# Performance work log

Measured on AMD Instinct MI355X. Metric: run time of the kernel, lower is better.

The kernel has to match this reference:

```python
import jax, jax.numpy as jnp
import numpy as np

D_STATE = 16
D_CONV = 4
EXPAND = 2
GROUPS = 8
EPS = 1e-5


def _layernorm(x, w, b):
    m = x.mean(-1, keepdims=True)
    v = x.var(-1, keepdims=True)
    return (x - m) * jax.lax.rsqrt(v + EPS) * w + b


def _groupnorm(x, w, b):
    B, C = x.shape[:2]
    sp = x.shape[2:]
    xg = x.reshape(B, GROUPS, C // GROUPS, -1)
    m = xg.mean(axis=(2, 3), keepdims=True)
    v = xg.var(axis=(2, 3), keepdims=True)
    xg = (xg - m) * jax.lax.rsqrt(v + EPS)
    x = xg.reshape((B, C) + sp)
    shp = (1, C) + (1,) * len(sp)
    return x * w.reshape(shp) + b.reshape(shp)


def _mamba(xn, in_w, conv_w, conv_b, xp_w, dt_w, dt_b, A_log, Dp, out_w):
    # xn: [B, L, C]
    B, L, C = xn.shape
    di = in_w.shape[0] // 2
    rank = dt_w.shape[1]
    N = D_STATE
    xz = xn @ in_w.T                              # [B, L, 2*di]
    xi, z = xz[..., :di], xz[..., di:]
    # causal depthwise conv1d along L (pad left d_conv-1, truncate to L)
    xc = jnp.moveaxis(xi, 1, 2)                   # [B, di, L]
    xpd = jnp.pad(xc, ((0, 0), (0, 0), (D_CONV - 1, 0)))
    conv = conv_b[None, :, None]
    for k in range(D_CONV):
        conv = conv + conv_w[None, :, k, None] * xpd[:, :, k:k + L]
    u = jnp.moveaxis(jax.nn.silu(conv), 1, 2)     # [B, L, di]
    dbl = u @ xp_w.T                              # [B, L, rank+2N]
    dt = dbl[..., :rank]
    Bm = dbl[..., rank:rank + N]
    Cm = dbl[..., rank + N:]
    delta = jax.nn.softplus(dt @ dt_w.T + dt_b)   # [B, L, di]
    A = -jnp.exp(A_log)                           # [di, N]
    dA = jnp.exp(delta[..., None] * A)            # [B, L, di, N]
    dBu = delta[..., None] * Bm[:, :, None, :] * u[..., None]

    def comb(e1, e2):
        a1, b1 = e1
        a2, b2 = e2
        return a1 * a2, a2 * b1 + b2

    _, h = jax.lax.associative_scan(comb, (dA, dBu), axis=1)  # h_t = dA_t*h_{t-1} + dBu_t
    y = jnp.einsum('bldn,bln->bld', h, Cm) + u * Dp
    y = y * jax.nn.silu(z)
    return y @ out_w.T


def _mamba_layer(x, p):
    B, C = x.shape[:2]
    img = x.shape[2:]
    L = int(np.prod(img))
    xf = jnp.moveaxis(x.reshape(B, C, L), 1, 2)   # [B, L, C]
    xn = _layernorm(xf, p['ln_w'], p['ln_b'])
    xm = _mamba(xn, p['in_w'], p['conv_w'], p['conv_b'], p['xp_w'],
                p['dt_w'], p['dt_b'], p['A_log'], p['Dp'], p['out_w'])
    xm = xm + p['skip'] * xf
    xm = _layernorm(xm, p['ln_w'], p['ln_b'])     # same norm params reused, as in source
    y = xm @ p['proj_w'].T + p['proj_b']
    return jnp.moveaxis(y, 1, 2).reshape((B, C) + img)


def setup_inputs() -> dict:
    key = jax.random.key(0)
    B, C = 2, 48
    img = (16, 32, 32)
    di = EXPAND * C
    rank = -(-C // 16)
    ks = iter(jax.random.split(key, 64))

    def nrm(shape, scale):
        return jax.random.normal(next(ks), shape, jnp.float32) * scale

    inp = {'x': jax.random.normal(next(ks), (B, C) + img, jnp.float32)}
    inp['gn1_w'] = jnp.ones(C); inp['gn1_b'] = jnp.zeros(C)
    inp['gn2_w'] = jnp.ones(C); inp['gn2_b'] = jnp.zeros(C)
    for i in (1, 2):
        inp[f'ln{i}_w'] = jnp.ones(C); inp[f'ln{i}_b'] = jnp.zeros(C)
        inp[f'in_w{i}'] = nrm((2 * di, C), C ** -0.5)
        inp[f'conv_w{i}'] = nrm((di, D_CONV), D_CONV ** -0.5)
        inp[f'conv_b{i}'] = jnp.zeros(di)
        inp[f'xp_w{i}'] = nrm((rank + 2 * D_STATE, di), di ** -0.5)
        inp[f'dt_w{i}'] = nrm((di, rank), rank ** -0.5)
        inp[f'dt_b{i}'] = nrm((di,), 0.1) - 4.0  # softplus -> small positive dt
        inp[f'A_log{i}'] = jnp.log(jnp.tile(jnp.arange(1, D_STATE + 1, dtype=jnp.float32), (di, 1)))
        inp[f'D{i}'] = jnp.ones(di)
        inp[f'out_w{i}'] = nrm((C, di), di ** -0.5)
        inp[f'proj_w{i}'] = nrm((C, C), C ** -0.5)
        inp[f'proj_b{i}'] = jnp.zeros(C)
        inp[f'skip{i}'] = jnp.ones(1)
    return inp


def reference(x, gn1_w, gn1_b, gn2_w, gn2_b,
              ln1_w, ln1_b, in_w1, conv_w1, conv_b1, xp_w1, dt_w1, dt_b1, A_log1, D1, out_w1, proj_w1, proj_b1, skip1,
              ln2_w, ln2_b, in_w2, conv_w2, conv_b2, xp_w2, dt_w2, dt_b2, A_log2, D2, out_w2, proj_w2, proj_b2, skip2):
    p1 = dict(ln_w=ln1_w, ln_b=ln1_b, in_w=in_w1, conv_w=conv_w1, conv_b=conv_b1, xp_w=xp_w1,
              dt_w=dt_w1, dt_b=dt_b1, A_log=A_log1, Dp=D1, out_w=out_w1, proj_w=proj_w1,
              proj_b=proj_b1, skip=skip1)
    p2 = dict(ln_w=ln2_w, ln_b=ln2_b, in_w=in_w2, conv_w=conv_w2, conv_b=conv_b2, xp_w=xp_w2,
              dt_w=dt_w2, dt_b=dt_b2, A_log=A_log2, Dp=D2, out_w=out_w2, proj_w=proj_w2,
              proj_b=proj_b2, skip=skip2)
    identity = x
    h = jax.nn.relu(_groupnorm(x, gn1_w, gn1_b))
    h = _mamba_layer(h, p1)
    h = jax.nn.relu(_groupnorm(h, gn2_w, gn2_b))
    h = _mamba_layer(h, p2)
    return h + identity
```

## Files before the change

### kernel.cpp

```cpp
#include <hip/hip_runtime.h>
#include <hip/hip_bf16.h>

#define LCH   48
#define DI    96
#define LSEQ  16384
#define NB    2
#define NPOS  (NB*LSEQ)
#define NSTATE 16
#define CPG   6
#define EPS   1e-5f
#define NC    128
#define CL    128
#define NCHAIN (NB*DI*NSTATE)
#define TS    32

typedef __hip_bfloat16 bf16;

__device__ __forceinline__ float LDW(const void* p, size_t i, bool f32){
    return f32 ? ((const float*)p)[i] : __bfloat162float(((const bf16*)p)[i]);
}

__device__ __forceinline__ float bf2f(unsigned short h){
    union { unsigned int i; float f; } u; u.i = ((unsigned int)h) << 16; return u.f;
}

__device__ __forceinline__ float4 LDW4(const void* p, size_t i4, bool f32){
    if (f32) return ((const float4*)p)[i4];
    ushort4 v = ((const ushort4*)p)[i4];
    return make_float4(bf2f(v.x), bf2f(v.y), bf2f(v.z), bf2f(v.w));
}

__device__ __forceinline__ float row16_sum(float p){
    union { float f; int i; } u, v;
    u.f = p; v.i = __builtin_amdgcn_mov_dpp(u.i, 0x111, 0xf, 0xf, true); p += v.f;
    u.f = p; v.i = __builtin_amdgcn_mov_dpp(u.i, 0x112, 0xf, 0xf, true); p += v.f;
    u.f = p; v.i = __builtin_amdgcn_mov_dpp(u.i, 0x114, 0xf, 0xf, true); p += v.f;
    u.f = p; v.i = __builtin_amdgcn_mov_dpp(u.i, 0x118, 0xf, 0xf, true); p += v.f;
    return p;
}

__global__ void k_flag(const void* gnw, int* flag){
    const unsigned short* g = (const unsigned short*)gnw;
    flag[0] = (g[0] == 0x3F80) ? 0 : 1;
}

__global__ void k_gnzero(float* __restrict__ acc){
    int t = threadIdx.x;
    if (t < 32) acc[t] = 0.f;
}

__global__ void k_gnpart_x(const void* __restrict__ x, const int* Fg, float* __restrict__ acc){
    const bool f32 = Fg[0];
    int bg = blockIdx.x >> 4, sl = blockIdx.x & 15;
    int b = bg >> 3, g = bg & 7;
    int tid = threadIdx.x;
    float s = 0.f, q = 0.f;
    for (int c = 0; c < CPG; ++c){
        size_t base = (size_t)(b*LCH + g*CPG + c)*LSEQ + sl*1024;
        for (int l = tid; l < 1024; l += 256){ float v = LDW(x, base + l, f32); s += v; q += v*v; }
    }
    __shared__ float ss[256], sq[256];
    ss[tid] = s; sq[tid] = q; __syncthreads();
    for (int st = 128; st > 0; st >>= 1){
        if (tid < st){ ss[tid] += ss[tid+st]; sq[tid] += sq[tid+st]; }
        __syncthreads();
    }
    if (tid == 0){
        atomicAdd(&acc[bg*2],   ss[0]);
        atomicAdd(&acc[bg*2+1], sq[0]);
    }
}

__global__ void k_gnpart_m(const float* __restrict__ m, float* __restrict__ acc){
    int bg = blockIdx.x >> 4, sl = blockIdx.x & 15;
    int b = bg >> 3, g = bg & 7;
    int tid = threadIdx.x;
    float s = 0.f, q = 0.f;
    for (int i = tid; i < 1024*CPG; i += 256){
        int l = sl*1024 + i/CPG, c = i % CPG;
        float v = m[(size_t)(b*LSEQ + l)*LCH + g*CPG + c];
        s += v; q += v*v;
    }
    __shared__ float ss[256], sq[256];
    ss[tid] = s; sq[tid] = q; __syncthreads();
    for (int st = 128; st > 0; st >>= 1){
        if (tid < st){ ss[tid] += ss[tid+st]; sq[tid] += sq[tid+st]; }
        __syncthreads();
    }
    if (tid == 0){
        atomicAdd(&acc[bg*2],   ss[0]);
        atomicAdd(&acc[bg*2+1], sq[0]);
    }
}

__global__ void k_gnfin(const float* __restrict__ acc, float* __restrict__ stats){
    int t = threadIdx.x;
    if (t < 16){
        float mean = acc[t*2] / (float)(CPG*LSEQ);
        float var  = acc[t*2+1] / (float)(CPG*LSEQ) - mean*mean;
        stats[t*2]   = mean;
        stats[t*2+1] = rsqrtf(var + EPS);
    }
}

__global__ void k_prep_x(const void* __restrict__ x, const int* Fg, const float* __restrict__ stats,
                         const void* gnw, const void* gnb, const void* lnw, const void* lnb,
                         float* __restrict__ xf, float* __restrict__ xn){
    const bool f32 = Fg[0];
    __shared__ float xl[128*49];
    __shared__ float fl[128*49];
    int tid = threadIdx.x;
    int pos0 = blockIdx.x*128;
    int b = pos0 >> 14, l0 = pos0 & (LSEQ-1);
    for (int i = tid; i < 48*128; i += 256){
        int c = i >> 7, p = i & 127;
        xl[p*49+c] = LDW(x, (size_t)(b*LCH+c)*LSEQ + l0 + p, f32);
    }
    __syncthreads();
    if (tid < 128){
        float* row  = xl + tid*49;
        float* frow = fl + tid*49;
        float s = 0.f, q = 0.f;
        #pragma unroll
        for (int c = 0; c < LCH; ++c){
            int g = c / CPG;
            float mean = stats[(b*8+g)*2], rs = stats[(b*8+g)*2+1];
            float v = row[c];
            v = (v - mean)*rs*LDW(gnw,c,f32) + LDW(gnb,c,f32);
            v = fmaxf(v, 0.f);
            frow[c] = v; s += v; q += v*v;
        }
        float mean = s / (float)LCH;
        float rs = rsqrtf(q/(float)LCH - mean*mean + EPS);
        #pragma unroll
        for (int c = 0; c < LCH; ++c)
            row[c] = (frow[c]-mean)*rs*LDW(lnw,c,f32) + LDW(lnb,c,f32);
    }
    __syncthreads();
    for (int i = tid; i < 128*48; i += 256){
        int p = i/48, c = i - p*48;
        xf[(size_t)pos0*LCH + i] = fl[p*49+c];
        xn[(size_t)pos0*LCH + i] = xl[p*49+c];
    }
}

__global__ void k_prep_m(const float* __restrict__ msrc, const int* Fg, const float* __restrict__ stats,
                         const void* gnw, const void* gnb, const void* lnw, const void* lnb,
                         float* __restrict__ xf, float* __restrict__ xn){
    const bool f32 = Fg[0];
    __shared__ float xl[128*49];
    __shared__ float fl[128*49];
    int tid = threadIdx.x;
    int pos0 = blockIdx.x*128;
    int b = pos0 >> 14;
    for (int i = tid; i < 128*48; i += 256){
        int p = i/48, c = i - p*48;
        xl[p*49+c] = msrc[(size_t)pos0*LCH + i];
    }
    __syncthreads();
    if (tid < 128){
        float* row  = xl + tid*49;
        float* frow = fl + tid*49;
        float s = 0.f, q = 0.f;
        #pragma unroll
        for (int c = 0; c < LCH; ++c){
            int g = c / CPG;
            float mean = stats[(b*8+g)*2], rs = stats[(b*8+g)*2+1];
            float v = row[c];
            v = (v - mean)*rs*LDW(gnw,c,f32) + LDW(gnb,c,f32);
            v = fmaxf(v, 0.f);
            frow[c] = v; s += v; q += v*v;
        }
        float mean = s / (float)LCH;
        float rs = rsqrtf(q/(float)LCH - mean*mean + EPS);
        #pragma unroll
        for (int c = 0; c < LCH; ++c)
            row[c] = (frow[c]-mean)*rs*LDW(lnw,c,f32) + LDW(lnb,c,f32);
    }
    __syncthreads();
    for (int i = tid; i < 128*48; i += 256){
        int p = i/48, c = i - p*48;
        xf[(size_t)pos0*LCH + i] = fl[p*49+c];
        xn[(size_t)pos0*LCH + i] = xl[p*49+c];
    }
}

__global__ void k_inproj(const float* __restrict__ xn, const void* __restrict__ inw, const int* Fg,
                         float* __restrict__ xi, float* __restrict__ z){
    const bool f32 = Fg[0];
    __shared__ float wl[192*50];
    __shared__ float xl[32*48];
    int pos0 = blockIdx.x*32;
    for (int i = threadIdx.x; i < 192*48; i += 256){
        int o = i/48, k = i - o*48;
        wl[o*50+k] = LDW(inw, i, f32);
    }
    for (int i = threadIdx.x; i < 32*48; i += 256)
        xl[i] = xn[(size_t)pos0*LCH + i];
    __syncthreads();
    int os = threadIdx.x & 63;
    int pofs = threadIdx.x >> 6;
    #pragma unroll
    for (int j = 0; j < 2; ++j){
        int p0 = pofs + j*16;
        float a0[4] = {0.f,0.f,0.f,0.f};
        float a1[4] = {0.f,0.f,0.f,0.f};
        float a2[4] = {0.f,0.f,0.f,0.f};
        #pragma unroll 4
        for (int k = 0; k < 48; ++k){
            float w0 = wl[ os      *50+k];
            float w1 = wl[(os+64 ) *50+k];
            float w2 = wl[(os+128) *50+k];
            #pragma unroll
            for (int q = 0; q < 4; ++q){
                float xv = xl[(p0+q*4)*48+k];
                a0[q] += xv*w0; a1[q] += xv*w1; a2[q] += xv*w2;
            }
        }
        #pragma unroll
        for (int q = 0; q < 4; ++q){
            int pos = pos0 + p0 + q*4;
            xi[(size_t)pos*DI + os] = a0[q];
            if (os < 32) xi[(size_t)pos*DI + 64 + os] = a1[q];
            else         z [(size_t)pos*DI + (os-32)] = a1[q];
            z[(size_t)pos*DI + (os+32)] = a2[q];
        }
    }
}

__global__ void k_convdbl(const float* __restrict__ xi, const void* cw, const void* cb,
                          const void* __restrict__ xpw, const void* dtw, const void* dtb,
                          const int* Fg, float* __restrict__ u_g, float* __restrict__ BC2,
                          float* __restrict__ delta_g){
    const bool f32 = Fg[0];
    __shared__ float xil[35*100];
    __shared__ float wbc[32*97];
    __shared__ float wdt[3*97];
    __shared__ float cwl[96*4];
    __shared__ float cbl[96];
    __shared__ float dtwl[96*3];
    __shared__ float dtbl[96];
    __shared__ float dtl[32*3];
    int tid = threadIdx.x;
    int pos0 = blockIdx.x*32;
    int l0 = pos0 & (LSEQ-1);

    for (int i = tid; i < 32*24; i += 256){
        int o = i/24, k4 = i - o*24;
        int row = (o & 1) ? (19 + (o>>1)) : (3 + (o>>1));
        float4 w = LDW4(xpw, (size_t)row*24 + k4, f32);
        wbc[o*97 + k4*4+0] = w.x; wbc[o*97 + k4*4+1] = w.y;
        wbc[o*97 + k4*4+2] = w.z; wbc[o*97 + k4*4+3] = w.w;
    }
    if (tid < 72){
        int o = tid/24, k4 = tid - o*24;
        float4 w = LDW4(xpw, (size_t)o*24 + k4, f32);
        wdt[o*97 + k4*4+0] = w.x; wdt[o*97 + k4*4+1] = w.y;
        wdt[o*97 + k4*4+2] = w.z; wdt[o*97 + k4*4+3] = w.w;
    }
    for (int i = tid; i < 96*4; i += 256) cwl[i] = LDW(cw, i, f32);
    if (tid < 96) cbl[tid] = LDW(cb, tid, f32);
    for (int i = tid; i < 96*3; i += 256) dtwl[i] = LDW(dtw, i, f32);
    if (tid >= 128 && tid < 224) dtbl[tid-128] = LDW(dtb, tid-128, f32);
    {
        float4* xv = (float4*)xil;
        const float4* gx = (const float4*)xi;
        for (int i = tid; i < 35*24; i += 256){
            int p = i/24, k4 = i - p*24;
            float4 v = make_float4(0.f, 0.f, 0.f, 0.f);
            if (l0 + p - 3 >= 0) v = gx[(size_t)(pos0-3+p)*24 + k4];
            xv[p*25 + k4] = v;
        }
    }
    __syncthreads();

    float uu[12];
    #pragma unroll
    for (int r = 0; r < 12; ++r){
        int i = tid + 256*r;
        int j = i/96, d = i - j*96;
        float acc = cbl[d];
        #pragma unroll
        for (int k = 0; k < 4; ++k)
            acc += cwl[d*4+k]*xil[(j+k)*100+d];
        uu[r] = acc / (1.f + __expf(-acc));
    }
    __syncthreads();

    #pragma unroll
    for (int r = 0; r < 12; ++r){
        int i = tid + 256*r;
        int j = i/96, d = i - j*96;
        xil[j*100+d] = uu[r];
        u_g[(size_t)pos0*DI + i] = uu[r];
    }
    __syncthreads();

    {
        int o  = tid & 31;
        int pg = ((tid>>6)<<1) | ((tid>>5)&1);
        const float4* ulv = (const float4*)xil;
        float a0=0.f, a1=0.f, a2=0.f, a3=0.f;
        #pragma unroll 4
        for (int k4 = 0; k4 < 24; ++k4){
            float4 u0 = ulv[(pg*4+0)*25 + k4];
            float4 u1 = ulv[(pg*4+1)*25 + k4];
            float4 u2 = ulv[(pg*4+2)*25 + k4];
            float4 u3 = ulv[(pg*4+3)*25 + k4];
            float w0 = wbc[o*97 + k4*4+0];
            float w1 = wbc[o*97 + k4*4+1];
            float w2 = wbc[o*97 + k4*4+2];
            float w3 = wbc[o*97 + k4*4+3];
            a0 += u0.x*w0; a0 += u0.y*w1; a0 += u0.z*w2; a0 += u0.w*w3;
            a1 += u1.x*w0; a1 += u1.y*w1; a1 += u1.z*w2; a1 += u1.w*w3;
            a2 += u2.x*w0; a2 += u2.y*w1; a2 += u2.z*w2; a2 += u2.w*w3;
            a3 += u3.x*w0; a3 += u3.y*w1; a3 += u3.z*w2; a3 += u3.w*w3;
        }
        size_t pb = (size_t)(pos0 + pg*4);
        BC2[(pb+0)*32 + o] = a0;
        BC2[(pb+1)*32 + o] = a1;
        BC2[(pb+2)*32 + o] = a2;
        BC2[(pb+3)*32 + o] = a3;
    }
    if (tid < 96){
        int o = tid >> 5;
        int p = tid & 31;
        const float4* ulv = (const float4*)xil;
        float a = 0.f;
        #pragma unroll 4
        for (int k4 = 0; k4 < 24; ++k4){
            float4 uv = ulv[p*25 + k4];
            a += uv.x*wdt[o*97 + k4*4+0];
            a += uv.y*wdt[o*97 + k4*4+1];
            a += uv.z*wdt[o*97 + k4*4+2];
            a += uv.w*wdt[o*97 + k4*4+3];
        }
        dtl[p*3+o] = a;
    }
    __syncthreads();

    for (int i = tid; i < 32*96; i += 256){
        int p = i/96, d = i - p*96;
        float acc = dtbl[d];
        #pragma unroll
        for (int r = 0; r < 3; ++r) acc += dtl[p*3+r]*dtwl[d*3+r];
        float sp = (acc > 20.f) ? acc : log1pf(__expf(acc));
        delta_g[(size_t)pos0*DI + i] = sp;
    }
}

__global__ void k_scanA(const float* __restrict__ delta, const float* __restrict__ u,
                        const float* __restrict__ BC2, const void* Alog, const int* Fg,
                        float* __restrict__ Pb, float* __restrict__ Sb){
    const bool f32 = Fg[0];
    __shared__ float  dls[2][TS*16];
    __shared__ float  uus[2][TS*16];
    __shared__ float2 bcs[2][TS*16];
    int tid = threadIdx.x;
    int t = blockIdx.x*256 + tid;
    int n = tid & 15;
    int sg0 = blockIdx.x*16;
    int cb2 = sg0/96;
    int d0 = sg0 - cb2*96;
    int b = cb2 & 1, chunk = cb2 >> 1;
    int dloc = tid >> 4;
    int d = d0 + dloc;
    float An = -__expf(LDW(Alog, d*16+n, f32));
    float P = 1.f, S = 0.f;
    int base = b*LSEQ + chunk*CL;
    const float2* BC2v = (const float2*)BC2;
    int si0 = tid >> 4, sj = tid & 15;
    int si1 = si0 + 16;
    float pd0, pd1, pu0, pu1; float2 pb0, pb1;
    auto fetch = [&](int tb){
        pd0 = delta[(size_t)(tb+si0)*DI + d0 + sj];
        pu0 = u    [(size_t)(tb+si0)*DI + d0 + sj];
        pb0 = BC2v [(size_t)(tb+si0)*16 + sj];
        pd1 = delta[(size_t)(tb+si1)*DI + d0 + sj];
        pu1 = u    [(size_t)(tb+si1)*DI + d0 + sj];
        pb1 = BC2v [(size_t)(tb+si1)*16 + sj];
    };
    auto store = [&](int bs){
        dls[bs][tid] = pd0; dls[bs][tid+256] = pd1;
        uus[bs][tid] = pu0; uus[bs][tid+256] = pu1;
        bcs[bs][tid] = pb0; bcs[bs][tid+256] = pb1;
    };
    fetch(base); store(0);
    __syncthreads();
    for (int tile = 0; tile < CL/TS; ++tile){
        int cur = tile & 1;
        if (tile+1 < CL/TS) fetch(base + (tile+1)*TS);
        #pragma unroll
        for (int i = 0; i < TS; ++i){
            float dl = dls[cur][i*16 + dloc];
            float uu = uus[cur][i*16 + dloc];
            float Bn = bcs[cur][i*16 + n].x;
            float a = __expf(dl*An);
            P *= a;
            S = a*S + dl*Bn*uu;
        }
        if (tile+1 < CL/TS) store(1-cur);
        __syncthreads();
    }
    Pb[t] = P; Sb[t] = S;
}

__global__ void k_scanB(const float* __restrict__ Pb, const float* __restrict__ Sb,
                        float* __restrict__ carry){
    int ch = blockIdx.x*blockDim.x + threadIdx.x;
    float c = 0.f;
    for (int cb = 0; cb < NC; cb += 8){
        float P[8], S[8];
        #pragma unroll
        for (int j = 0; j < 8; ++j){
            P[j] = Pb[(size_t)(cb+j)*NCHAIN + ch];
            S[j] = Sb[(size_t)(cb+j)*NCHAIN + ch];
        }
        #pragma unroll
        for (int j = 0; j < 8; ++j){
            carry[(size_t)(cb+j)*NCHAIN + ch] = c;
            c = S[j] + P[j]*c;
        }
    }
}

__global__ void k_scanC(const float* __restrict__ delta, const float* __restrict__ u,
                        const float* __restrict__ BC2, const float* __restrict__ carry,
                        const void* Alog, const int* Fg, float* __restrict__ y){
    const bool f32 = Fg[0];
    __shared__ float  dls[2][TS*16];
    __shared__ float  uus[2][TS*16];
    __shared__ float2 bcs[2][TS*16];
    int tid = threadIdx.x;
    int n = tid & 15;
    int sg0 = blockIdx.x*16;
    int cb2 = sg0/96;
    int d0 = sg0 - cb2*96;
    int b = cb2 & 1, chunk = cb2 >> 1;
    int dloc = tid >> 4;
    int d = d0 + dloc;
    float An = -__expf(LDW(Alog, d*16+n, f32));
    float h = carry[chunk*NCHAIN + (b*DI+d)*NSTATE + n];
    int base = b*LSEQ + chunk*CL;
    const float2* BC2v = (const float2*)BC2;
    int si0 = tid >> 4, sj = tid & 15;
    int si1 = si0 + 16;
    float pd0, pd1, pu0, pu1; float2 pb0, pb1;
    auto fetch = [&](int tb){
        pd0 = delta[(size_t)(tb+si0)*DI + d0 + sj];
        pu0 = u    [(size_t)(tb+si0)*DI + d0 + sj];
        pb0 = BC2v [(size_t)(tb+si0)*16 + sj];
        pd1 = delta[(size_t)(tb+si1)*DI + d0 + sj];
        pu1 = u    [(size_t)(tb+si1)*DI + d0 + sj];
        pb1 = BC2v [(size_t)(tb+si1)*16 + sj];
    };
    auto store = [&](int bs){
        dls[bs][tid] = pd0; dls[bs][tid+256] = pd1;
        uus[bs][tid] = pu0; uus[bs][tid+256] = pu1;
        bcs[bs][tid] = pb0; bcs[bs][tid+256] = pb1;
    };
    fetch(base); store(0);
    __syncthreads();
    for (int tile = 0; tile < CL/TS; ++tile){
        int cur = tile & 1;
        int tb = base + tile*TS;
        if (tile+1 < CL/TS) fetch(base + (tile+1)*TS);
        #pragma unroll
        for (int i = 0; i < TS; ++i){
            float dl = dls[cur][i*16 + dloc];
            float uu = uus[cur][i*16 + dloc];
            float2 bc = bcs[cur][i*16 + n];
            float a = __expf(dl*An);
            h = a*h + dl*bc.x*uu;
            float p = row16_sum(h*bc.y);
            if (n == 15) y[(size_t)(tb+i)*DI + d] = p;
        }
        if (tile+1 < CL/TS) store(1-cur);
        __syncthreads();
    }
}

__global__ void k_outproj(const float* __restrict__ psum, const void* __restrict__ outw,
                          const void* skipv, const void* Dp, const int* Fg,
                          const float* __restrict__ u, const float* __restrict__ zx,
                          const float* __restrict__ xf, float* __restrict__ xm){
    const bool f32 = Fg[0];
    __shared__ float wl[48*98];
    __shared__ float yl[32*96];
    int pos0 = blockIdx.x*32;
    for (int i = threadIdx.x; i < 48*96; i += 256){
        int o = i/96, k = i - o*96;
        wl[o*98+k] = LDW(outw, i, f32);
    }
    for (int i = threadIdx.x; i < 32*96; i += 256){
        int d = i % DI;
        float pv = psum[(size_t)pos0*DI + i];
        float uu = u   [(size_t)pos0*DI + i];
        float zz = zx  [(size_t)pos0*DI + i];
        float yv = pv + uu*LDW(Dp, d, f32);
        yl[i] = yv * (zz / (1.f + __expf(-zz)));
    }
    __syncthreads();
    float sk = LDW(skipv, 0, f32);
    int os = threadIdx.x & 63;
    int pofs = threadIdx.x >> 6;
    #pragma unroll
    for (int j = 0; j < 2; ++j){
        int p0 = pofs + j*16;
        float a[4] = {0.f,0.f,0.f,0.f};
        if (os < 48){
            #pragma unroll 4
            for (int k = 0; k < 96; ++k){
                float w = wl[os*98+k];
                #pragma unroll
                for (int q = 0; q < 4; ++q)
                    a[q] += yl[(p0+q*4)*96+k]*w;
            }
            #pragma unroll
            for (int q = 0; q < 4; ++q){
                size_t oi = (size_t)(pos0+p0+q*4)*LCH + os;
                xm[oi] = a[q] + sk*xf[oi];
            }
        }
    }
}

__global__ void k_lnproj(const float* __restrict__ xm, const void* lnw, const void* lnb,
                         const void* __restrict__ pw, const void* pb, const int* Fg,
                         float* __restrict__ m){
    const bool f32 = Fg[0];
    __shared__ float wl[48*50];
    __shared__ float xl[32*49];
    int pos0 = blockIdx.x*32;
    for (int i = threadIdx.x; i < 48*48; i += 256){
        int o = i/48, k = i - o*48;
        wl[o*50+k] = LDW(pw, i, f32);
    }
    for (int i = threadIdx.x; i < 32*48; i += 256){
        int p = i/48, c = i - p*48;
        xl[p*49+c] = xm[(size_t)pos0*LCH + i];
    }
    __syncthreads();
    if (threadIdx.x < 32){
        float* row = xl + threadIdx.x*49;
        float s = 0.f, q = 0.f;
        #pragma unroll
        for (int c = 0; c < LCH; ++c){ float v = row[c]; s += v; q += v*v; }
        float mean = s / (float)LCH;
        float rs = rsqrtf(q/(float)LCH - mean*mean + EPS);
        #pragma unroll
        for (int c = 0; c < LCH; ++c)
            row[c] = (row[c]-mean)*rs*LDW(lnw,c,f32) + LDW(lnb,c,f32);
    }
    __syncthreads();
    int os = threadIdx.x & 63;
    int pofs = threadIdx.x >> 6;
    float bias = (os < 48) ? LDW(pb, os, f32) : 0.f;
    #pragma unroll
    for (int j = 0; j < 2; ++j){
        int p0 = pofs + j*16;
        float a[4];
        #pragma unroll
        for (int q = 0; q < 4; ++q) a[q] = bias;
        if (os < 48){
            #pragma unroll 4
            for (int k = 0; k < 48; ++k){
                float w = wl[os*50+k];
                #pragma unroll
                for (int q = 0; q < 4; ++q)
                    a[q] += xl[(p0+q*4)*49+k]*w;
            }
            #pragma unroll
            for (int q = 0; q < 4; ++q)
                m[(size_t)(pos0+p0+q*4)*LCH + os] = a[q];
        }
    }
}

__global__ void k_final(const float* __restrict__ m, const void* __restrict__ x, const int* Fg,
                        void* __restrict__ out){
    const bool f32 = Fg[0];
    __shared__ float ml[128*49];
    int tid = threadIdx.x;
    int pos0 = blockIdx.x*128;
    int b = pos0 >> 14, l0 = pos0 & (LSEQ-1);
    for (int i = tid; i < 128*48; i += 256){
        int p = i/48, c = i - p*48;
        ml[p*49+c] = m[(size_t)pos0*LCH + i];
    }
    __syncthreads();
    for (int i = tid; i < 48*128; i += 256){
        int c = i >> 7, p = i & 127;
        size_t gi = (size_t)(b*LCH+c)*LSEQ + l0 + p;
        float v = ml[p*49+c] + LDW(x, gi, f32);
        if (f32) ((float*)out)[gi] = v;
        else     ((bf16*)out)[gi] = __float2bfloat16(v);
    }
}

extern "C" void kernel_launch(void* const* d_in, const int* in_sizes, int n_in,
                              void* d_out, int out_size, void* d_ws, size_t ws_size,
                              hipStream_t stream){
    const void* x = d_in[0];
    auto W = [&](int i){ return (const void*)d_in[i]; };

    float* ws = (float*)d_ws;
    size_t off = 0;
    int*   flag  = (int*)ws;  off += 16;
    float* stats = ws + off;  off += 64;
    float* gacc  = ws + off;  off += 32;
    float* xf    = ws + off;  off += (size_t)NPOS*LCH;
    float* xn    = ws + off;  off += (size_t)NPOS*LCH;
    float* xi    = ws + off;  off += (size_t)NPOS*DI;
    float* zb    = ws + off;  off += (size_t)NPOS*DI;
    float* ub    = ws + off;  off += (size_t)NPOS*DI;
    size_t scan0 = off;
    float* dt3   = ws + off;  off += (size_t)NPOS*3;
    float* BC2   = ws + off;  off += (size_t)NPOS*32;
    float* Pb    = ws + off;  off += (size_t)NC*NCHAIN;
    float* Sb    = ws + off;  off += (size_t)NC*NCHAIN;
    float* carry = ws + off;  off += (size_t)NC*NCHAIN;
    float* delta = ws + off;  off += (size_t)NPOS*DI;
    float* mbuf  = ws + off;  off += (size_t)NPOS*LCH;
    float* ybuf  = xi;
    float* xmbuf = ws + scan0;
    (void)dt3;

    k_flag<<<1, 1, 0, stream>>>(W(1), flag);

    k_gnzero<<<1, 64, 0, stream>>>(gacc);
    k_gnpart_x<<<256, 256, 0, stream>>>(x, flag, gacc);
    k_gnfin<<<1, 16, 0, stream>>>(gacc, stats);
    k_prep_x<<<NPOS/128, 256, 0, stream>>>(x, flag, stats, W(1), W(2), W(5), W(6), xf, xn);
    k_inproj<<<NPOS/32, 256, 0, stream>>>(xn, W(7), flag, xi, zb);
    k_convdbl<<<NPOS/32, 256, 0, stream>>>(xi, W(8), W(9), W(10), W(11), W(12), flag, ub, BC2, delta);
    k_scanA<<<NC*NCHAIN/256, 256, 0, stream>>>(delta, ub, BC2, W(13), flag, Pb, Sb);
    k_scanB<<<NCHAIN/256, 256, 0, stream>>>(Pb, Sb, carry);
    k_scanC<<<NC*NCHAIN/256, 256, 0, stream>>>(delta, ub, BC2, carry, W(13), flag, ybuf);
    k_outproj<<<NPOS/32, 256, 0, stream>>>(ybuf, W(15), W(18), W(14), flag, ub, zb, xf, xmbuf);
    k_lnproj<<<NPOS/32, 256, 0, stream>>>(xmbuf, W(5), W(6), W(16), W(17), flag, mbuf);

    k_gnzero<<<1, 64, 0, stream>>>(gacc);
    k_gnpart_m<<<256, 256, 0, stream>>>(mbuf, gacc);
    k_gnfin<<<1, 16, 0, stream>>>(gacc, stats);
    k_prep_m<<<NPOS/128, 256, 0, stream>>>(mbuf, flag, stats, W(3), W(4), W(19), W(20), xf, xn);
    k_inproj<<<NPOS/32, 256, 0, stream>>>(xn, W(21), flag, xi, zb);
    k_convdbl<<<NPOS/32, 256, 0, stream>>>(xi, W(22), W(23), W(24), W(25), W(26), flag, ub, BC2, delta);
    k_scanA<<<NC*NCHAIN/256, 256, 0, stream>>>(delta, ub, BC2, W(27), flag, Pb, Sb);
    k_scanB<<<NCHAIN/256, 256, 0, stream>>>(Pb, Sb, carry);
    k_scanC<<<NC*NCHAIN/256, 256, 0, stream>>>(delta, ub, BC2, carry, W(27), flag, ybuf);
    k_outproj<<<NPOS/32, 256, 0, stream>>>(ybuf, W(29), W(32), W(28), flag, ub, zb, xf, xmbuf);
    k_lnproj<<<NPOS/32, 256, 0, stream>>>(xmbuf, W(19), W(20), W(30), W(31), flag, mbuf);

    k_final<<<NPOS/128, 256, 0, stream>>>(mbuf, x, flag, d_out);
}
```

Baseline: 511.4 us.

## Fuse norm, projections, groupnorm stats and residual into fewer kernels

Folds flag setup and accumulator zeroing into one kernel, and moves the groupnorm finalisation plus groupnorm/layernorm prep into the in-projection kernel. Out-projection, layernorm and the linear projection become one kernel, which also accumulates the next groupnorm's statistics or writes the final residual output. This removes several launches and the round trips of the xn, xm and m intermediates through global memory. In exchange each block uses more shared memory, prep runs on only 32 threads per 32-position block, and statistics now go through shared and global atomics.

```diff
diff --git a/kernel.cpp b/kernel.cpp
--- a/kernel.cpp
+++ b/kernel.cpp
@@ -39,14 +39,13 @@
     return p;
 }
 
-__global__ void k_flag(const void* gnw, int* flag){
-    const unsigned short* g = (const unsigned short*)gnw;
-    flag[0] = (g[0] == 0x3F80) ? 0 : 1;
-}
-
-__global__ void k_gnzero(float* __restrict__ acc){
+__global__ void k_flag(const void* gnw, int* flag, float* __restrict__ acc1, float* __restrict__ acc2){
     int t = threadIdx.x;
-    if (t < 32) acc[t] = 0.f;
+    if (t == 0){
+        const unsigned short* g = (const unsigned short*)gnw;
+        flag[0] = (g[0] == 0x3F80) ? 0 : 1;
+    }
+    if (t < 32){ acc1[t] = 0.f; acc2[t] = 0.f; }
 }
 
 __global__ void k_gnpart_x(const void* __restrict__ x, const int* Fg, float* __restrict__ acc){
@@ -57,7 +56,11 @@
     float s = 0.f, q = 0.f;
     for (int c = 0; c < CPG; ++c){
         size_t base = (size_t)(b*LCH + g*CPG + c)*LSEQ + sl*1024;
-        for (int l = tid; l < 1024; l += 256){ float v = LDW(x, base + l, f32); s += v; q += v*v; }
+        float4 v = LDW4(x, base/4 + tid, f32);
+        s += v.x; q += v.x*v.x;
+        s += v.y; q += v.y*v.y;
+        s += v.z; q += v.z*v.z;
+        s += v.w; q += v.w*v.w;
     }
     __shared__ float ss[256], sq[256];
     ss[tid] = s; sq[tid] = q; __syncthreads();
@@ -71,60 +74,50 @@
     }
 }
 
-__global__ void k_gnpart_m(const float* __restrict__ m, float* __restrict__ acc){
-    int bg = blockIdx.x >> 4, sl = blockIdx.x & 15;
-    int b = bg >> 3, g = bg & 7;
+template<int SRC>
+__global__ void k_prepin(const void* __restrict__ src, const int* Fg, const float* __restrict__ acc,
+                         const void* gnw, const void* gnb, const void* lnw, const void* lnb,
+                         const void* __restrict__ inw,
+                         float* __restrict__ xf, float* __restrict__ xi, float* __restrict__ z){
+    const bool f32 = Fg[0];
+    __shared__ float wl[192*49];
+    __shared__ float xl[32*49];
+    __shared__ float fl[32*49];
+    __shared__ float sst[32];
     int tid = threadIdx.x;
-    float s = 0.f, q = 0.f;
-    for (int i = tid; i < 1024*CPG; i += 256){
-        int l = sl*1024 + i/CPG, c = i % CPG;
-        float v = m[(size_t)(b*LSEQ + l)*LCH + g*CPG + c];
-        s += v; q += v*v;
-    }
-    __shared__ float ss[256], sq[256];
-    ss[tid] = s; sq[tid] = q; __syncthreads();
-    for (int st = 128; st > 0; st >>= 1){
-        if (tid < st){ ss[tid] += ss[tid+st]; sq[tid] += sq[tid+st]; }
-        __syncthreads();
-    }
-    if (tid == 0){
-        atomicAdd(&acc[bg*2],   ss[0]);
-        atomicAdd(&acc[bg*2+1], sq[0]);
-    }
-}
-
-__global__ void k_gnfin(const float* __restrict__ acc, float* __restrict__ stats){
-    int t = threadIdx.x;
-    if (t < 16){
-        float mean = acc[t*2] / (float)(CPG*LSEQ);
-        float var  = acc[t*2+1] / (float)(CPG*LSEQ) - mean*mean;
-        stats[t*2]   = mean;
-        stats[t*2+1] = rsqrtf(var + EPS);
-    }
-}
-
-__global__ void k_prep_x(const void* __restrict__ x, const int* Fg, const float* __restrict__ stats,
-                         const void* gnw, const void* gnb, const void* lnw, const void* lnb,
-                         float* __restrict__ xf, float* __restrict__ xn){
-    const bool f32 = Fg[0];
-    __shared__ float xl[128*49];
-    __shared__ float fl[128*49];
-    int tid = threadIdx.x;
-    int pos0 = blockIdx.x*128;
+    int pos0 = blockIdx.x*32;
     int b = pos0 >> 14, l0 = pos0 & (LSEQ-1);
-    for (int i = tid; i < 48*128; i += 256){
-        int c = i >> 7, p = i & 127;
-        xl[p*49+c] = LDW(x, (size_t)(b*LCH+c)*LSEQ + l0 + p, f32);
-    }
-    __syncthreads();
-    if (tid < 128){
+    if (tid < 16){
+        float mean = acc[tid*2] / (float)(CPG*LSEQ);
+        float var  = acc[tid*2+1] / (float)(CPG*LSEQ) - mean*mean;
+        sst[tid*2]   = mean;
+        sst[tid*2+1] = rsqrtf(var + EPS);
+    }
+    for (int i = tid; i < 192*48; i += 256){
+        int o = i/48, k = i - o*48;
+        wl[o*49+k] = LDW(inw, i, f32);
+    }
+    if (SRC == 0){
+        for (int i = tid; i < 48*32; i += 256){
+            int c = i >> 5, p = i & 31;
+            xl[p*49+c] = LDW(src, (size_t)(b*LCH+c)*LSEQ + l0 + p, f32);
+        }
+    } else {
+        const float* ms = (const float*)src;
+        for (int i = tid; i < 32*48; i += 256){
+            int p = i/48, c = i - p*48;
+            xl[p*49+c] = ms[(size_t)pos0*LCH + i];
+        }
+    }
+    __syncthreads();
+    if (tid < 32){
         float* row  = xl + tid*49;
         float* frow = fl + tid*49;
         float s = 0.f, q = 0.f;
         #pragma unroll
         for (int c = 0; c < LCH; ++c){
             int g = c / CPG;
-            float mean = stats[(b*8+g)*2], rs = stats[(b*8+g)*2+1];
+            float mean = sst[(b*8+g)*2], rs = sst[(b*8+g)*2+1];
             float v = row[c];
             v = (v - mean)*rs*LDW(gnw,c,f32) + LDW(gnb,c,f32);
             v = fmaxf(v, 0.f);
@@ -137,69 +130,12 @@
             row[c] = (frow[c]-mean)*rs*LDW(lnw,c,f32) + LDW(lnb,c,f32);
     }
     __syncthreads();
-    for (int i = tid; i < 128*48; i += 256){
+    for (int i = tid; i < 32*48; i += 256){
         int p = i/48, c = i - p*48;
         xf[(size_t)pos0*LCH + i] = fl[p*49+c];
-        xn[(size_t)pos0*LCH + i] = xl[p*49+c];
-    }
-}
-
-__global__ void k_prep_m(const float* __restrict__ msrc, const int* Fg, const float* __restrict__ stats,
-                         const void* gnw, const void* gnb, const void* lnw, const void* lnb,
-                         float* __restrict__ xf, float* __restrict__ xn){
-    const bool f32 = Fg[0];
-    __shared__ float xl[128*49];
-    __shared__ float fl[128*49];
-    int tid = threadIdx.x;
-    int pos0 = blockIdx.x*128;
-    int b = pos0 >> 14;
-    for (int i = tid; i < 128*48; i += 256){
-        int p = i/48, c = i - p*48;
-        xl[p*49+c] = msrc[(size_t)pos0*LCH + i];
-    }
-    __syncthreads();
-    if (tid < 128){
-        float* row  = xl + tid*49;
-        float* frow = fl + tid*49;
-        float s = 0.f, q = 0.f;
-        #pragma unroll
-        for (int c = 0; c < LCH; ++c){
-            int g = c / CPG;
-            float mean = stats[(b*8+g)*2], rs = stats[(b*8+g)*2+1];
-            float v = row[c];
-            v = (v - mean)*rs*LDW(gnw,c,f32) + LDW(gnb,c,f32);
-            v = fmaxf(v, 0.f);
-            frow[c] = v; s += v; q += v*v;
-        }
-        float mean = s / (float)LCH;
-        float rs = rsqrtf(q/(float)LCH - mean*mean + EPS);
-        #pragma unroll
-        for (int c = 0; c < LCH; ++c)
-            row[c] = (frow[c]-mean)*rs*LDW(lnw,c,f32) + LDW(lnb,c,f32);
-    }
-    __syncthreads();
-    for (int i = tid; i < 128*48; i += 256){
-        int p = i/48, c = i - p*48;
-        xf[(size_t)pos0*LCH + i] = fl[p*49+c];
-        xn[(size_t)pos0*LCH + i] = xl[p*49+c];
-    }
-}
-
-__global__ void k_inproj(const float* __restrict__ xn, const void* __restrict__ inw, const int* Fg,
-                         float* __restrict__ xi, float* __restrict__ z){
-    const bool f32 = Fg[0];
-    __shared__ float wl[192*50];
-    __shared__ float xl[32*48];
-    int pos0 = blockIdx.x*32;
-    for (int i = threadIdx.x; i < 192*48; i += 256){
-        int o = i/48, k = i - o*48;
-        wl[o*50+k] = LDW(inw, i, f32);
-    }
-    for (int i = threadIdx.x; i < 32*48; i += 256)
-        xl[i] = xn[(size_t)pos0*LCH + i];
-    __syncthreads();
-    int os = threadIdx.x & 63;
-    int pofs = threadIdx.x >> 6;
+    }
+    int os = tid & 63;
+    int pofs = tid >> 6;
     #pragma unroll
     for (int j = 0; j < 2; ++j){
         int p0 = pofs + j*16;
@@ -208,12 +144,12 @@
         float a2[4] = {0.f,0.f,0.f,0.f};
         #pragma unroll 4
         for (int k = 0; k < 48; ++k){
-            float w0 = wl[ os      *50+k];
-            float w1 = wl[(os+64 ) *50+k];
-            float w2 = wl[(os+128) *50+k];
+            float w0 = wl[ os      *49+k];
+            float w1 = wl[(os+64 ) *49+k];
+            float w2 = wl[(os+128) *49+k];
             #pragma unroll
             for (int q = 0; q < 4; ++q){
-                float xv = xl[(p0+q*4)*48+k];
+                float xv = xl[(p0+q*4)*49+k];
                 a0[q] += xv*w0; a1[q] += xv*w1; a2[q] += xv*w2;
             }
         }
@@ -480,19 +416,33 @@
     }
 }
 
-__global__ void k_outproj(const float* __restrict__ psum, const void* __restrict__ outw,
-                          const void* skipv, const void* Dp, const int* Fg,
-                          const float* __restrict__ u, const float* __restrict__ zx,
-                          const float* __restrict__ xf, float* __restrict__ xm){
+template<int FIN>
+__global__ void k_outln(const float* __restrict__ psum, const void* __restrict__ outw,
+                        const void* skipv, const void* Dp, const int* Fg,
+                        const float* __restrict__ u, const float* __restrict__ zx,
+                        const float* __restrict__ xf,
+                        const void* lnw, const void* lnb,
+                        const void* __restrict__ pw, const void* pb,
+                        const void* __restrict__ xres, float* __restrict__ mout,
+                        float* __restrict__ acc2, void* __restrict__ outp){
     const bool f32 = Fg[0];
-    __shared__ float wl[48*98];
+    __shared__ float wl[48*97];
     __shared__ float yl[32*96];
+    __shared__ float wp[48*49];
+    __shared__ float xmr[32*49];
+    __shared__ float gs[48], gq[48];
+    int tid = threadIdx.x;
     int pos0 = blockIdx.x*32;
-    for (int i = threadIdx.x; i < 48*96; i += 256){
+    if (FIN == 0 && tid < 48){ gs[tid] = 0.f; gq[tid] = 0.f; }
+    for (int i = tid; i < 48*96; i += 256){
         int o = i/96, k = i - o*96;
-        wl[o*98+k] = LDW(outw, i, f32);
-    }
-    for (int i = threadIdx.x; i < 32*96; i += 256){
+        wl[o*97+k] = LDW(outw, i, f32);
+    }
+    for (int i = tid; i < 48*48; i += 256){
+        int o = i/48, k = i - o*48;
+        wp[o*49+k] = LDW(pw, i, f32);
+    }
+    for (int i = tid; i < 32*96; i += 256){
         int d = i % DI;
         float pv = psum[(size_t)pos0*DI + i];
         float uu = u   [(size_t)pos0*DI + i];
@@ -502,8 +452,8 @@
     }
     __syncthreads();
     float sk = LDW(skipv, 0, f32);
-    int os = threadIdx.x & 63;
-    int pofs = threadIdx.x >> 6;
+    int os = tid & 63;
+    int pofs = tid >> 6;
     #pragma unroll
     for (int j = 0; j < 2; ++j){
         int p0 = pofs + j*16;
@@ -511,38 +461,22 @@
         if (os < 48){
             #pragma unroll 4
             for (int k = 0; k < 96; ++k){
-                float w = wl[os*98+k];
+                float w = wl[os*97+k];
                 #pragma unroll
                 for (int q = 0; q < 4; ++q)
                     a[q] += yl[(p0+q*4)*96+k]*w;
             }
             #pragma unroll
             for (int q = 0; q < 4; ++q){
-                size_t oi = (size_t)(pos0+p0+q*4)*LCH + os;
-                xm[oi] = a[q] + sk*xf[oi];
+                int p = p0 + q*4;
+                size_t oi = (size_t)(pos0+p)*LCH + os;
+                xmr[p*49+os] = a[q] + sk*xf[oi];
             }
         }
     }
-}
-
-__global__ void k_lnproj(const float* __restrict__ xm, const void* lnw, const void* lnb,
-                         const void* __restrict__ pw, const void* pb, const int* Fg,
-                         float* __restrict__ m){
-    const bool f32 = Fg[0];
-    __shared__ float wl[48*50];
-    __shared__ float xl[32*49];
-    int pos0 = blockIdx.x*32;
-    for (int i = threadIdx.x; i < 48*48; i += 256){
-        int o = i/48, k = i - o*48;
-        wl[o*50+k] = LDW(pw, i, f32);
-    }
-    for (int i = threadIdx.x; i < 32*48; i += 256){
-        int p = i/48, c = i - p*48;
-        xl[p*49+c] = xm[(size_t)pos0*LCH + i];
-    }
-    __syncthreads();
-    if (threadIdx.x < 32){
-        float* row = xl + threadIdx.x*49;
+    __syncthreads();
+    if (tid < 32){
+        float* row = xmr + tid*49;
         float s = 0.f, q = 0.f;
         #pragma unroll
         for (int c = 0; c < LCH; ++c){ float v = row[c]; s += v; q += v*v; }
@@ -553,9 +487,8 @@
             row[c] = (row[c]-mean)*rs*LDW(lnw,c,f32) + LDW(lnb,c,f32);
     }
     __syncthreads();
-    int os = threadIdx.x & 63;
-    int pofs = threadIdx.x >> 6;
     float bias = (os < 48) ? LDW(pb, os, f32) : 0.f;
+    float sl = 0.f, ql = 0.f;
     #pragma unroll
     for (int j = 0; j < 2; ++j){
         int p0 = pofs + j*16;
@@ -565,36 +498,43 @@
         if (os < 48){
             #pragma unroll 4
             for (int k = 0; k < 48; ++k){
-                float w = wl[os*50+k];
+                float w = wp[os*49+k];
                 #pragma unroll
                 for (int q = 0; q < 4; ++q)
-                    a[q] += xl[(p0+q*4)*49+k]*w;
+                    a[q] += xmr[(p0+q*4)*49+k]*w;
             }
             #pragma unroll
-            for (int q = 0; q < 4; ++q)
-                m[(size_t)(pos0+p0+q*4)*LCH + os] = a[q];
-        }
-    }
-}
-
-__global__ void k_final(const float* __restrict__ m, const void* __restrict__ x, const int* Fg,
-                        void* __restrict__ out){
-    const bool f32 = Fg[0];
-    __shared__ float ml[128*49];
-    int tid = threadIdx.x;
-    int pos0 = blockIdx.x*128;
-    int b = pos0 >> 14, l0 = pos0 & (LSEQ-1);
-    for (int i = tid; i < 128*48; i += 256){
-        int p = i/48, c = i - p*48;
-        ml[p*49+c] = m[(size_t)pos0*LCH + i];
-    }
-    __syncthreads();
-    for (int i = tid; i < 48*128; i += 256){
-        int c = i >> 7, p = i & 127;
-        size_t gi = (size_t)(b*LCH+c)*LSEQ + l0 + p;
-        float v = ml[p*49+c] + LDW(x, gi, f32);
-        if (f32) ((float*)out)[gi] = v;
-        else     ((bf16*)out)[gi] = __float2bfloat16(v);
+            for (int q = 0; q < 4; ++q){
+                if (FIN == 0){
+                    mout[(size_t)(pos0+p0+q*4)*LCH + os] = a[q];
+                    sl += a[q]; ql += a[q]*a[q];
+                } else {
+                    yl[(p0+q*4)*49 + os] = a[q];
+                }
+            }
+        }
+    }
+    if (FIN == 0){
+        if (os < 48){ atomicAdd(&gs[os], sl); atomicAdd(&gq[os], ql); }
+        __syncthreads();
+        if (tid < 8){
+            int b = pos0 >> 14;
+            float s = 0.f, q = 0.f;
+            #pragma unroll
+            for (int c = 0; c < CPG; ++c){ s += gs[tid*CPG+c]; q += gq[tid*CPG+c]; }
+            atomicAdd(&acc2[(b*8+tid)*2],   s);
+            atomicAdd(&acc2[(b*8+tid)*2+1], q);
+        }
+    } else {
+        __syncthreads();
+        int b = pos0 >> 14, l0 = pos0 & (LSEQ-1);
+        for (int i = tid; i < 48*32; i += 256){
+            int c = i >> 5, p = i & 31;
+            size_t gi = (size_t)(b*LCH+c)*LSEQ + l0 + p;
+            float v = yl[p*49+c] + LDW(xres, gi, f32);
+            if (f32) ((float*)outp)[gi] = v;
+            else     ((bf16*)outp)[gi] = __float2bfloat16(v);
+        }
     }
 }
 
@@ -607,15 +547,12 @@
     float* ws = (float*)d_ws;
     size_t off = 0;
     int*   flag  = (int*)ws;  off += 16;
-    float* stats = ws + off;  off += 64;
-    float* gacc  = ws + off;  off += 32;
+    float* acc1  = ws + off;  off += 32;
+    float* acc2  = ws + off;  off += 32;
     float* xf    = ws + off;  off += (size_t)NPOS*LCH;
-    float* xn    = ws + off;  off += (size_t)NPOS*LCH;
     float* xi    = ws + off;  off += (size_t)NPOS*DI;
     float* zb    = ws + off;  off += (size_t)NPOS*DI;
     float* ub    = ws + off;  off += (size_t)NPOS*DI;
-    size_t scan0 = off;
-    float* dt3   = ws + off;  off += (size_t)NPOS*3;
     float* BC2   = ws + off;  off += (size_t)NPOS*32;
     float* Pb    = ws + off;  off += (size_t)NC*NCHAIN;
     float* Sb    = ws + off;  off += (size_t)NC*NCHAIN;
@@ -623,34 +560,23 @@
     float* delta = ws + off;  off += (size_t)NPOS*DI;
     float* mbuf  = ws + off;  off += (size_t)NPOS*LCH;
     float* ybuf  = xi;
-    float* xmbuf = ws + scan0;
-    (void)dt3;
-
-    k_flag<<<1, 1, 0, stream>>>(W(1), flag);
-
-    k_gnzero<<<1, 64, 0, stream>>>(gacc);
-    k_gnpart_x<<<256, 256, 0, stream>>>(x, flag, gacc);
-    k_gnfin<<<1, 16, 0, stream>>>(gacc, stats);
-    k_prep_x<<<NPOS/128, 256, 0, stream>>>(x, flag, stats, W(1), W(2), W(5), W(6), xf, xn);
-    k_inproj<<<NPOS/32, 256, 0, stream>>>(xn, W(7), flag, xi, zb);
+
+    k_flag<<<1, 64, 0, stream>>>(W(1), flag, acc1, acc2);
+
+    k_gnpart_x<<<256, 256, 0, stream>>>(x, flag, acc1);
+    k_prepin<0><<<NPOS/32, 256, 0, stream>>>(x, flag, acc1, W(1), W(2), W(5), W(6), W(7), xf, xi, zb);
     k_convdbl<<<NPOS/32, 256, 0, stream>>>(xi, W(8), W(9), W(10), W(11), W(12), flag, ub, BC2, delta);
     k_scanA<<<NC*NCHAIN/256, 256, 0, stream>>>(delta, ub, BC2, W(13), flag, Pb, Sb);
     k_scanB<<<NCHAIN/256, 256, 0, stream>>>(Pb, Sb, carry);
     k_scanC<<<NC*NCHAIN/256, 256, 0, stream>>>(delta, ub, BC2, carry, W(13), flag, ybuf);
-    k_outproj<<<NPOS/32, 256, 0, stream>>>(ybuf, W(15), W(18), W(14), flag, ub, zb, xf, xmbuf);
-    k_lnproj<<<NPOS/32, 256, 0, stream>>>(xmbuf, W(5), W(6), W(16), W(17), flag, mbuf);
-
-    k_gnzero<<<1, 64, 0, stream>>>(gacc);
-    k_gnpart_m<<<256, 256, 0, stream>>>(mbuf, gacc);
-    k_gnfin<<<1, 16, 0, stream>>>(gacc, stats);
-    k_prep_m<<<NPOS/128, 256, 0, stream>>>(mbuf, flag, stats, W(3), W(4), W(19), W(20), xf, xn);
-    k_inproj<<<NPOS/32, 256, 0, stream>>>(xn, W(21), flag, xi, zb);
+    k_outln<0><<<NPOS/32, 256, 0, stream>>>(ybuf, W(15), W(18), W(14), flag, ub, zb, xf,
+                                            W(5), W(6), W(16), W(17), nullptr, mbuf, acc2, nullptr);
+
+    k_prepin<1><<<NPOS/32, 256, 0, stream>>>(mbuf, flag, acc2, W(3), W(4), W(19), W(20), W(21), xf, xi, zb);
     k_convdbl<<<NPOS/32, 256, 0, stream>>>(xi, W(22), W(23), W(24), W(25), W(26), flag, ub, BC2, delta);
     k_scanA<<<NC*NCHAIN/256, 256, 0, stream>>>(delta, ub, BC2, W(27), flag, Pb, Sb);
     k_scanB<<<NCHAIN/256, 256, 0, stream>>>(Pb, Sb, carry);
     k_scanC<<<NC*NCHAIN/256, 256, 0, stream>>>(delta, ub, BC2, carry, W(27), flag, ybuf);
-    k_outproj<<<NPOS/32, 256, 0, stream>>>(ybuf, W(29), W(32), W(28), flag, ub, zb, xf, xmbuf);
-    k_lnproj<<<NPOS/32, 256, 0, stream>>>(xmbuf, W(19), W(20), W(30), W(31), flag, mbuf);
-
-    k_final<<<NPOS/128, 256, 0, stream>>>(mbuf, x, flag, d_out);
-}
+    k_outln<1><<<NPOS/32, 256, 0, stream>>>(ybuf, W(29), W(32), W(28), flag, ub, zb, xf,
+                                            W(19), W(20), W(30), W(31), x, nullptr, nullptr, d_out);
+}
```

Result: no change. 521.1 us (+1.9%).
